# Optimization experiments

Measured on AMD Instinct MI355X. Metric: run time of the kernel, lower is better.

Reference implementation:

```python
import jax, jax.numpy as jnp
import numpy as np

HEADS = 16

def _split_heads(t, h):
    # 'b y (h d) -> (b h) y d'
    b, y, hd = t.shape
    d = hd // h
    return t.reshape(b, y, h, d).transpose(0, 2, 1, 3).reshape(b * h, y, d)

def _merge_heads(t, b, h):
    # '(b h) y d -> b y (h d)'
    bh, y, d = t.shape
    return t.reshape(b, h, y, d).transpose(0, 2, 1, 3).reshape(b, y, h * d)

def setup_inputs() -> dict:
    key = jax.random.key(0)
    ks = jax.random.split(key, 5)
    B, S, D = 8, 4096, 1024
    scale = 1.0 / np.sqrt(D)
    x = jax.random.normal(ks[0], (B, S, D), dtype=jnp.float32)
    Wq = jax.random.normal(ks[1], (D, D), dtype=jnp.float32) * scale
    Wk = jax.random.normal(ks[2], (D, D), dtype=jnp.float32) * scale
    Wv = jax.random.normal(ks[3], (D, D), dtype=jnp.float32) * scale
    Wo = jax.random.normal(ks[4], (D, D), dtype=jnp.float32) * scale
    return {"x": x, "Wq": Wq, "Wk": Wk, "Wv": Wv, "Wo": Wo}

def reference(x, Wq, Wk, Wv, Wo):
    b = x.shape[0]
    h = HEADS
    # torch nn.Linear stores weight as (out, in): y = x @ W.T
    q = _split_heads(x @ Wq.T, h)  # (b*h, y, d)
    k = _split_heads(x @ Wk.T, h)
    v = _split_heads(x @ Wv.T, h)
    d = q.shape[-1]
    # NOTE: faithfully contracts over the sequence axis y -> (b*h, d, d) scores
    z = jnp.einsum('byq,byk->bkq', q, k) / jnp.sqrt(jnp.asarray(d, x.dtype))
    z = jax.nn.softmax(z, axis=-1)
    z = jnp.einsum('byz,bvy->bvz', z, v)  # (b*h, seq, d)
    z = _merge_heads(z, b, h)             # (b, seq, h*d)
    # output projection (dropout is identity in eval)
    return z @ Wo.T
```

## Files before the change

kernel.cpp:

```cpp
#include <hip/hip_runtime.h>
#include <hip/hip_fp16.h>

typedef _Float16 f16;
typedef _Float16 f16x8 __attribute__((ext_vector_type(8)));
typedef _Float16 f16x4 __attribute__((ext_vector_type(4)));
typedef float    f32x4 __attribute__((ext_vector_type(4)));

#define MFMA16(a, b, c) __builtin_amdgcn_mfma_f32_16x16x32_f16((a), (b), (c), 0, 0, 0)

#define BARR() __builtin_amdgcn_s_barrier()
#define VMW4() asm volatile("s_waitcnt vmcnt(4)" ::: "memory")
#define VMW0() asm volatile("s_waitcnt vmcnt(0)" ::: "memory")
#define LGKM0() asm volatile("s_waitcnt lgkmcnt(0)" ::: "memory")
#define SB0()  __builtin_amdgcn_sched_barrier(0)

#define GLOAD16(P, L)                                                          \
  __builtin_amdgcn_global_load_lds(                                            \
      (const __attribute__((address_space(1))) unsigned int*)(P),              \
      (__attribute__((address_space(3))) unsigned int*)(L), 16, 0, 0)

__global__ __launch_bounds__(256) void cast_f32_to_f16(const float* __restrict__ src,
                                                       f16* __restrict__ dst, int n4) {
  int i = blockIdx.x * 256 + threadIdx.x;
  if (i >= n4) return;
  float4 v = reinterpret_cast<const float4*>(src)[i];
  f16x4 o = { (f16)v.x, (f16)v.y, (f16)v.z, (f16)v.w };
  reinterpret_cast<f16x4*>(dst)[i] = o;
}

template <typename OutT>
__global__ __launch_bounds__(512, 1) void gemm_bt_8ph(const f16* __restrict__ A,
                                                      const f16* __restrict__ B,
                                                      OutT* __restrict__ C,
                                                      int N, int nby) {
  constexpr int K = 1024;
  __shared__ f16 lds[2][2][2][8192];

  const int tid = threadIdx.x;
  const int wid = tid >> 6, l = tid & 63;
  const int wr = wid >> 2, wc = wid & 3;

  const int nwg = gridDim.x;
  const int cpx = nwg >> 3;
  const int id = blockIdx.x;
  const int swz = (id & 7) * cpx + (id >> 3);
  const int by = swz % nby, bx = swz / nby;

  int r0s, c0s, r1s, c1s;
  {
    int rel = tid * 16;
    int sub = rel >> 10, q = rel & 1023;
    int inner = q ^ (((q >> 9) & 1) << 5);
    r0s = ((sub >> 1) << 4) + (inner >> 6);
    c0s = ((sub & 1) << 5) + ((inner & 63) >> 1);
    rel = (512 + tid) * 16;
    sub = rel >> 10; q = rel & 1023;
    inner = q ^ (((q >> 9) & 1) << 5);
    r1s = ((sub >> 1) << 4) + (inner >> 6);
    c1s = ((sub & 1) << 5) + ((inner & 63) >> 1);
  }
  const f16* gA0a = A + (size_t)(by * 256 + r0s) * K + c0s;
  const f16* gA0b = A + (size_t)(by * 256 + r1s) * K + c1s;
  const f16* gA1a = gA0a + 128 * K;
  const f16* gA1b = gA0b + 128 * K;
  const f16* gB0a = B + (size_t)(bx * 256 + r0s) * K + c0s;
  const f16* gB0b = B + (size_t)(bx * 256 + r1s) * K + c1s;
  const f16* gB1a = gB0a + 128 * K;
  const f16* gB1b = gB0b + 128 * K;

#define STAGE_P(G0, G1, EOFF, LB, MAT, H)                                      \
  { GLOAD16((G0) + (EOFF), &lds[LB][MAT][H][wid * 512]);                       \
    GLOAD16((G1) + (EOFF), &lds[LB][MAT][H][4096 + wid * 512]); }

  const int lane_rd = (((l & 15) << 6) + ((l >> 4) << 4)) ^ (((l >> 3) & 1) << 5);
  const char* rdA0 = (const char*)&lds[0][0][wr][0] + lane_rd;
  const char* rdA1 = (const char*)&lds[1][0][wr][0] + lane_rd;
  const char* rdB0 = (const char*)&lds[0][1][wc >> 1][0] + (wc & 1) * 8192 + lane_rd;
  const char* rdB1 = (const char*)&lds[1][1][wc >> 1][0] + (wc & 1) * 8192 + lane_rd;

  f16x8 af[4][2], bf0[2][2], bf1[2][2];
  f32x4 acc[8][4] = {};

#define READ_A_MH(RD, mh)                                                      \
  _Pragma("unroll") for (int mm = 0; mm < 4; ++mm)                             \
  _Pragma("unroll") for (int ks = 0; ks < 2; ++ks)                             \
    af[mm][ks] = *reinterpret_cast<const f16x8*>(                              \
        (RD) + (((((mh)*4 + mm) * 2) + ks) << 10));
#define READ_B_NH(DST, RD, nh)                                                 \
  _Pragma("unroll") for (int nn = 0; nn < 2; ++nn)                             \
  _Pragma("unroll") for (int ks = 0; ks < 2; ++ks)                             \
    DST[nn][ks] = *reinterpret_cast<const f16x8*>(                             \
        (RD) + (((((nh)*2 + nn) * 2) + ks) << 10));
#define CL2(BF, mh, nh)                                                        \
  __builtin_amdgcn_s_setprio(1);                                               \
  _Pragma("unroll") for (int mm = 0; mm < 4; ++mm)                             \
  _Pragma("unroll") for (int nn = 0; nn < 2; ++nn)                             \
  _Pragma("unroll") for (int ks = 0; ks < 2; ++ks)                             \
    acc[(mh)*4 + mm][(nh)*2 + nn] =                                            \
        MFMA16(af[mm][ks], BF[nn][ks], acc[(mh)*4 + mm][(nh)*2 + nn]);         \
  __builtin_amdgcn_s_setprio(0);

  STAGE_P(gB0a, gB0b, 0, 0, 1, 0);
  STAGE_P(gB1a, gB1b, 0, 0, 1, 1);
  STAGE_P(gA0a, gA0b, 0, 0, 0, 0);
  STAGE_P(gA1a, gA1b, 0, 0, 0, 1);
  STAGE_P(gB0a, gB0b, 64, 1, 1, 0);
  STAGE_P(gB1a, gB1b, 64, 1, 1, 1);
  VMW4();
  BARR();

  for (int i = 0; i < 8; ++i) {
    const bool more = (i < 7);
    READ_A_MH(rdA0, 0); READ_B_NH(bf0, rdB0, 0);
    STAGE_P(gA0a, gA0b, 64, 1, 0, 0);
    BARR(); LGKM0(); SB0(); CL2(bf0, 0, 0); BARR();
    READ_B_NH(bf1, rdB0, 1);
    STAGE_P(gA1a, gA1b, 64, 1, 0, 1);
    BARR(); LGKM0(); SB0(); CL2(bf1, 0, 1); BARR();
    READ_A_MH(rdA0, 1);
    if (more) STAGE_P(gB0a, gB0b, 128, 0, 1, 0);
    BARR(); LGKM0(); SB0(); CL2(bf1, 1, 1); BARR();
    if (more) STAGE_P(gB1a, gB1b, 128, 0, 1, 1);
    BARR(); SB0(); CL2(bf0, 1, 0);
    if (more) { VMW4(); } else { VMW0(); }
    BARR();
    READ_A_MH(rdA1, 0); READ_B_NH(bf0, rdB1, 0);
    if (more) STAGE_P(gA0a, gA0b, 128, 0, 0, 0);
    BARR(); LGKM0(); SB0(); CL2(bf0, 0, 0); BARR();
    READ_B_NH(bf1, rdB1, 1);
    if (more) STAGE_P(gA1a, gA1b, 128, 0, 0, 1);
    BARR(); LGKM0(); SB0(); CL2(bf1, 0, 1); BARR();
    READ_A_MH(rdA1, 1);
    if (more) STAGE_P(gB0a, gB0b, 192, 1, 1, 0);
    BARR(); LGKM0(); SB0(); CL2(bf1, 1, 1); BARR();
    if (more) STAGE_P(gB1a, gB1b, 192, 1, 1, 1);
    BARR(); SB0(); CL2(bf0, 1, 0);
    if (more) VMW4();
    BARR();
    gA0a += 128; gA0b += 128; gA1a += 128; gA1b += 128;
    gB0a += 128; gB0b += 128; gB1a += 128; gB1b += 128;
  }

  const int rr = by * 256 + wr * 128 + ((l >> 4) << 2);
  const int cc = bx * 256 + wc * 64 + (l & 15);
#pragma unroll
  for (int m = 0; m < 8; ++m)
#pragma unroll
    for (int n = 0; n < 4; ++n)
#pragma unroll
      for (int j = 0; j < 4; ++j)
        C[(size_t)(rr + m * 16 + j) * N + cc + n * 16] = (OutT)acc[m][n][j];
#undef STAGE_P
#undef READ_A_MH
#undef READ_B_NH
#undef CL2
}

__global__ __launch_bounds__(256, 2) void scores_part(const f16* __restrict__ qkv,
                                                      float* __restrict__ part) {
  const int seg = blockIdx.x;
  const int bh = blockIdx.y;
  const int b = bh >> 4, h = bh & 15;
  const f16* qg = qkv + (size_t)b * 4096 * 3072 + h * 64;
  const f16* kg = qg + 1024;

  __shared__ f16 sQ[64 * 72];
  __shared__ f16 sK[64 * 72];

  const int tid = threadIdx.x;
  const int w = tid >> 6, l = tid & 63;

  f32x4 acc[4] = {};

  const int yb = seg * 256;
  for (int y0 = yb; y0 < yb + 256; y0 += 64) {
    __syncthreads();
#pragma unroll
    for (int cc = 0; cc < 2; ++cc) {
      const int c = 2 * w + cc;
      f16x8 vq = *reinterpret_cast<const f16x8*>(qg + (size_t)(y0 + l) * 3072 + c * 8);
      f16x8 vk = *reinterpret_cast<const f16x8*>(kg + (size_t)(y0 + l) * 3072 + c * 8);
#pragma unroll
      for (int j = 0; j < 8; ++j) {
        sQ[(c * 8 + j) * 72 + l] = vq[j];
        sK[(c * 8 + j) * 72 + l] = vk[j];
      }
    }
    __syncthreads();
#pragma unroll
    for (int ks = 0; ks < 2; ++ks) {
      f16x8 a = *reinterpret_cast<const f16x8*>(sK + (w * 16 + (l & 15)) * 72 + ks * 32 + ((l >> 4) << 3));
#pragma unroll
      for (int n = 0; n < 4; ++n) {
        f16x8 bq = *reinterpret_cast<const f16x8*>(sQ + (n * 16 + (l & 15)) * 72 + ks * 32 + ((l >> 4) << 3));
        acc[n] = MFMA16(a, bq, acc[n]);
      }
    }
  }

  float* dst = part + ((size_t)(bh * 16 + seg)) * 4096;
#pragma unroll
  for (int n = 0; n < 4; ++n)
#pragma unroll
    for (int j = 0; j < 4; ++j)
      dst[(w * 16 + ((l >> 4) << 2) + j) * 64 + n * 16 + (l & 15)] = acc[n][j] * 0.125f;
}

__global__ __launch_bounds__(64) void scores_combine(const float* __restrict__ part,
                                                     f16* __restrict__ zt) {
  const int bh = blockIdx.x;
  const int kd = threadIdx.x;
  float s[64];
#pragma unroll
  for (int q = 0; q < 64; ++q) s[q] = 0.f;
  const float* p0 = part + (size_t)bh * 16 * 4096 + kd * 64;
  for (int seg = 0; seg < 16; ++seg) {
    const float4* ps = reinterpret_cast<const float4*>(p0 + seg * 4096);
#pragma unroll
    for (int q4 = 0; q4 < 16; ++q4) {
      float4 v = ps[q4];
      s[q4 * 4 + 0] += v.x; s[q4 * 4 + 1] += v.y;
      s[q4 * 4 + 2] += v.z; s[q4 * 4 + 3] += v.w;
    }
  }
  float mx = -1e30f;
#pragma unroll
  for (int q = 0; q < 64; ++q) mx = fmaxf(mx, s[q]);
  float sum = 0.f;
#pragma unroll
  for (int q = 0; q < 64; ++q) { float e = __expf(s[q] - mx); s[q] = e; sum += e; }
  float inv = 1.f / sum;
  f16* dst = zt + (size_t)bh * 4096 + kd;
#pragma unroll
  for (int q = 0; q < 64; ++q) dst[q * 64] = (f16)(s[q] * inv);
}

__global__ __launch_bounds__(256, 2) void pv_merge(const f16* __restrict__ qkv,
                                                   const f16* __restrict__ zt,
                                                   f16* __restrict__ out2) {
  const int st = blockIdx.x;
  const int bh = blockIdx.y;
  const int b = bh >> 4, h = bh & 15;
  const f16* vg = qkv + (size_t)(b * 4096 + st * 128) * 3072 + 2048 + h * 64;

  __shared__ f16 sV[128 * 72];
  __shared__ f16 sZ[64 * 72];

  const int tid = threadIdx.x;
  const int w = tid >> 6, l = tid & 63;

#pragma unroll
  for (int p = 0; p < 4; ++p) {
    int idx = (p * 256 + tid) * 8;
    int row = idx >> 6, col = idx & 63;
    f16x8 v = *reinterpret_cast<const f16x8*>(vg + (size_t)row * 3072 + col);
    *reinterpret_cast<f16x8*>(sV + row * 72 + col) = v;
  }
#pragma unroll
  for (int p = 0; p < 2; ++p) {
    int idx = (p * 256 + tid) * 8;
    int row = idx >> 6, col = idx & 63;
    f16x8 v = *reinterpret_cast<const f16x8*>(zt + (size_t)bh * 4096 + idx);
    *reinterpret_cast<f16x8*>(sZ + row * 72 + col) = v;
  }
  __syncthreads();

  f32x4 acc[2][4] = {};
#pragma unroll
  for (int ks = 0; ks < 2; ++ks) {
    f16x8 av[2], bz[4];
#pragma unroll
    for (int m = 0; m < 2; ++m)
      av[m] = *reinterpret_cast<const f16x8*>(sV + (w * 32 + m * 16 + (l & 15)) * 72 + ks * 32 + ((l >> 4) << 3));
#pragma unroll
    for (int n = 0; n < 4; ++n)
      bz[n] = *reinterpret_cast<const f16x8*>(sZ + (n * 16 + (l & 15)) * 72 + ks * 32 + ((l >> 4) << 3));
#pragma unroll
    for (int m = 0; m < 2; ++m)
#pragma unroll
      for (int n = 0; n < 4; ++n)
        acc[m][n] = MFMA16(av[m], bz[n], acc[m][n]);
  }

#pragma unroll
  for (int m = 0; m < 2; ++m)
#pragma unroll
    for (int n = 0; n < 4; ++n)
#pragma unroll
      for (int j = 0; j < 4; ++j) {
        int s = st * 128 + w * 32 + m * 16 + ((l >> 4) << 2) + j;
        out2[(size_t)(b * 4096 + s) * 1024 + h * 64 + n * 16 + (l & 15)] = (f16)acc[m][n][j];
      }
}

extern "C" void kernel_launch(void* const* d_in, const int* in_sizes, int n_in,
                              void* d_out, int out_size, void* d_ws, size_t ws_size,
                              hipStream_t stream) {
  const float* x  = (const float*)d_in[0];
  const float* Wq = (const float*)d_in[1];
  const float* Wk = (const float*)d_in[2];
  const float* Wv = (const float*)d_in[3];
  const float* Wo = (const float*)d_in[4];
  float* out = (float*)d_out;

  f16* xh    = (f16*)d_ws;
  f16* qkvh  = xh + 33554432;
  f16* wqkvh = qkvh + 100663296;
  f16* woh   = wqkvh + 3145728;
  f16* zth   = woh + 1048576;
  f16* out2h = zth + 524288;
  float* part = (float*)d_ws;

  cast_f32_to_f16<<<32768, 256, 0, stream>>>(x, xh, 33554432 / 4);
  cast_f32_to_f16<<<1024, 256, 0, stream>>>(Wq, wqkvh, 1048576 / 4);
  cast_f32_to_f16<<<1024, 256, 0, stream>>>(Wk, wqkvh + 1048576, 1048576 / 4);
  cast_f32_to_f16<<<1024, 256, 0, stream>>>(Wv, wqkvh + 2097152, 1048576 / 4);
  cast_f32_to_f16<<<1024, 256, 0, stream>>>(Wo, woh, 1048576 / 4);

  gemm_bt_8ph<f16><<<128 * 12, 512, 0, stream>>>(xh, wqkvh, qkvh, 3072, 128);

  scores_part<<<dim3(16, 128), 256, 0, stream>>>(qkvh, part);
  scores_combine<<<128, 64, 0, stream>>>(part, zth);

  pv_merge<<<dim3(32, 128), 256, 0, stream>>>(qkvh, zth, out2h);

  gemm_bt_8ph<float><<<128 * 4, 512, 0, stream>>>(out2h, woh, out, 1024, 128);
}
```

Measured before the change: 425.7 us.

## Deepen GEMM A-tile prefetch and restructure scores kernel global loads

Measured after the change: 415.6 us. 1.02x faster.

```diff
diff --git a/kernel.cpp b/kernel.cpp
--- a/kernel.cpp
+++ b/kernel.cpp
@@ -9,6 +9,7 @@
 #define MFMA16(a, b, c) __builtin_amdgcn_mfma_f32_16x16x32_f16((a), (b), (c), 0, 0, 0)
 
 #define BARR() __builtin_amdgcn_s_barrier()
+#define VMW6() asm volatile("s_waitcnt vmcnt(6)" ::: "memory")
 #define VMW4() asm volatile("s_waitcnt vmcnt(4)" ::: "memory")
 #define VMW0() asm volatile("s_waitcnt vmcnt(0)" ::: "memory")
 #define LGKM0() asm volatile("s_waitcnt lgkmcnt(0)" ::: "memory")
@@ -106,16 +107,16 @@
   STAGE_P(gA1a, gA1b, 0, 0, 0, 1);
   STAGE_P(gB0a, gB0b, 64, 1, 1, 0);
   STAGE_P(gB1a, gB1b, 64, 1, 1, 1);
-  VMW4();
+  STAGE_P(gA0a, gA0b, 64, 1, 0, 0);
+  VMW6();
   BARR();
 
   for (int i = 0; i < 8; ++i) {
     const bool more = (i < 7);
     READ_A_MH(rdA0, 0); READ_B_NH(bf0, rdB0, 0);
-    STAGE_P(gA0a, gA0b, 64, 1, 0, 0);
+    STAGE_P(gA1a, gA1b, 64, 1, 0, 1);
     BARR(); LGKM0(); SB0(); CL2(bf0, 0, 0); BARR();
     READ_B_NH(bf1, rdB0, 1);
-    STAGE_P(gA1a, gA1b, 64, 1, 0, 1);
     BARR(); LGKM0(); SB0(); CL2(bf1, 0, 1); BARR();
     READ_A_MH(rdA0, 1);
     if (more) STAGE_P(gB0a, gB0b, 128, 0, 1, 0);
@@ -133,9 +134,9 @@
     READ_A_MH(rdA1, 1);
     if (more) STAGE_P(gB0a, gB0b, 192, 1, 1, 0);
     BARR(); LGKM0(); SB0(); CL2(bf1, 1, 1); BARR();
-    if (more) STAGE_P(gB1a, gB1b, 192, 1, 1, 1);
+    if (more) { STAGE_P(gB1a, gB1b, 192, 1, 1, 1); STAGE_P(gA0a, gA0b, 192, 1, 0, 0); }
     BARR(); SB0(); CL2(bf0, 1, 0);
-    if (more) VMW4();
+    if (more) VMW6();
     BARR();
     gA0a += 128; gA0b += 128; gA1a += 128; gA1b += 128;
     gB0a += 128; gB0b += 128; gB1a += 128; gB1b += 128;
@@ -161,30 +162,37 @@
   const int seg = blockIdx.x;
   const int bh = blockIdx.y;
   const int b = bh >> 4, h = bh & 15;
-  const f16* qg = qkv + (size_t)b * 4096 * 3072 + h * 64;
-  const f16* kg = qg + 1024;
+  const f16* base = qkv + (size_t)b * 4096 * 3072 + h * 64;
 
   __shared__ f16 sQ[64 * 72];
   __shared__ f16 sK[64 * 72];
 
   const int tid = threadIdx.x;
   const int w = tid >> 6, l = tid & 63;
+
+  const int tsel = w >> 1;
+  const int g = ((w & 1) << 6) + l;
+  const int row = g >> 1;
+  const int ch = g & 1;
+  const f16* src = base + tsel * 1024 + (size_t)row * 3072 + ch * 32;
+  f16* dstL = (tsel ? sK : sQ) + (ch * 32) * 72 + row;
 
   f32x4 acc[4] = {};
 
   const int yb = seg * 256;
   for (int y0 = yb; y0 < yb + 256; y0 += 64) {
     __syncthreads();
-#pragma unroll
-    for (int cc = 0; cc < 2; ++cc) {
-      const int c = 2 * w + cc;
-      f16x8 vq = *reinterpret_cast<const f16x8*>(qg + (size_t)(y0 + l) * 3072 + c * 8);
-      f16x8 vk = *reinterpret_cast<const f16x8*>(kg + (size_t)(y0 + l) * 3072 + c * 8);
-#pragma unroll
-      for (int j = 0; j < 8; ++j) {
-        sQ[(c * 8 + j) * 72 + l] = vq[j];
-        sK[(c * 8 + j) * 72 + l] = vk[j];
-      }
+    const f16* s0 = src + (size_t)y0 * 3072;
+    f16x8 v0 = *reinterpret_cast<const f16x8*>(s0);
+    f16x8 v1 = *reinterpret_cast<const f16x8*>(s0 + 8);
+    f16x8 v2 = *reinterpret_cast<const f16x8*>(s0 + 16);
+    f16x8 v3 = *reinterpret_cast<const f16x8*>(s0 + 24);
+#pragma unroll
+    for (int j = 0; j < 8; ++j) {
+      dstL[j * 72] = v0[j];
+      dstL[(8 + j) * 72] = v1[j];
+      dstL[(16 + j) * 72] = v2[j];
+      dstL[(24 + j) * 72] = v3[j];
     }
     __syncthreads();
 #pragma unroll
```
